# Kernel optimization log

Hardware: AMD Instinct MI355X
Metric: run time of the kernel (lower is better)

## Reference

```python
import jax, jax.numpy as jnp
import numpy as np

B, T, D = 2, 2048, 2048
H = 16
NOPE, ROPE = 128, 64
Q_HEAD = NOPE + ROPE            # 192
Q_LORA = H * Q_HEAD // 4        # 768
KV_RANK = 512
V_DIM = 128
EPS = 1e-6


def setup_inputs() -> dict:
    key = jax.random.key(0)
    ks = jax.random.split(key, 8)
    s = lambda k, shape: jax.random.normal(k, shape, dtype=jnp.float32) * (1.0 / np.sqrt(shape[0]))
    return {
        "hidden_states": jax.random.normal(ks[0], (B, T, D), dtype=jnp.float32),
        "positions": jnp.broadcast_to(jnp.arange(T, dtype=jnp.int64 if jax.config.jax_enable_x64 else jnp.int32), (B, T)),
        "w_qa": s(ks[1], (D, Q_LORA)),
        "g_qa": jnp.ones((Q_LORA,), jnp.float32),
        "w_qb": s(ks[2], (Q_LORA, H * Q_HEAD)),
        "w_kva": s(ks[3], (D, KV_RANK + ROPE)),
        "g_kva": jnp.ones((KV_RANK,), jnp.float32),
        "w_kvb": s(ks[4], (KV_RANK, H * (NOPE + V_DIM))),
        "w_o": s(ks[5], (H * V_DIM, D)),
    }


def _rms(x, g):
    return x * jax.lax.rsqrt(jnp.mean(x * x, axis=-1, keepdims=True) + EPS) * g


def _rotate_half(x):
    h = x.shape[-1] // 2
    return jnp.concatenate([-x[..., h:], x[..., :h]], axis=-1)


def _rope_tables(n):
    inv_freq = 1.0 / (10000.0 ** (jnp.arange(0, ROPE, 2, dtype=jnp.float32) / ROPE))
    freqs = jnp.arange(n, dtype=jnp.float32)[:, None] * inv_freq[None, :]
    emb = jnp.concatenate([freqs, freqs], axis=-1)  # [n, ROPE]
    return jnp.cos(emb), jnp.sin(emb)


def reference(hidden_states, positions, w_qa, g_qa, w_qb, w_kva, g_kva, w_kvb, w_o):
    Bq, Tq, _ = hidden_states.shape
    # Q: low-rank down-proj + RMSNorm + up-proj
    q = _rms(hidden_states @ w_qa, g_qa) @ w_qb
    q = q.reshape(Bq, Tq, H, Q_HEAD)
    q_nope, q_rope = q[..., :NOPE], q[..., NOPE:]
    # KV compression (prefill: no past cache, S == T)
    kvc = hidden_states @ w_kva
    new_c_kv = _rms(kvc[..., :KV_RANK], g_kva)     # [B,S,rank]
    new_k_rope = kvc[..., KV_RANK:]                # [B,S,ROPE]
    S = new_c_kv.shape[1]
    kv = (new_c_kv @ w_kvb).reshape(Bq, S, H, NOPE + V_DIM)
    k_nope, v = kv[..., :NOPE], kv[..., NOPE:]
    # Decoupled RoPE on the rope sub-dimension only
    cos_full, sin_full = _rope_tables(S)
    cos_q = cos_full[positions][:, :, None, :]     # [B,T,1,ROPE]
    sin_q = sin_full[positions][:, :, None, :]
    q_rope = q_rope * cos_q + _rotate_half(q_rope) * sin_q
    cos_k = cos_full[None, :, :]                   # [1,S,ROPE] (all_positions = arange(S))
    sin_k = sin_full[None, :, :]
    k_rope = new_k_rope * cos_k + _rotate_half(new_k_rope) * sin_k  # [B,S,ROPE], shared across heads
    # Assemble full q/k, attention
    q_full = jnp.concatenate([q_nope, q_rope], axis=-1).transpose(0, 2, 1, 3)  # [B,H,T,192]
    k_full = jnp.concatenate(
        [k_nope, jnp.broadcast_to(k_rope[:, :, None, :], (Bq, S, H, ROPE))], axis=-1
    ).transpose(0, 2, 1, 3)                                                     # [B,H,S,192]
    v = v.transpose(0, 2, 1, 3)                                                 # [B,H,S,Vd]
    scale = Q_HEAD ** -0.5
    attn = jnp.einsum("bhtd,bhsd->bhts", q_full, k_full) * scale
    row = jnp.arange(Tq)[:, None]
    col = jnp.arange(S)[None, :]
    attn = jnp.where(col > row + (S - Tq), -jnp.inf, attn)
    attn = jax.nn.softmax(attn, axis=-1)
    out = jnp.einsum("bhts,bhsd->bhtd", attn, v)
    out = out.transpose(0, 2, 1, 3).reshape(Bq, Tq, H * V_DIM)
    output = out @ w_o
    return output, new_c_kv, new_k_rope
```

## Files before the change

### kernel.cpp

```cpp
#include <hip/hip_runtime.h>
#include <stdint.h>

typedef unsigned short ushort_t;
typedef ushort_t u16x8 __attribute__((ext_vector_type(8)));
typedef short s16x8 __attribute__((ext_vector_type(8)));
typedef float f32x4 __attribute__((ext_vector_type(4)));

#define B_ 2
#define T_ 2048
#define D_ 2048
#define H_ 16
#define NOPE_ 128
#define ROPE_ 64
#define QHEAD_ 192
#define QLORA_ 768
#define KVRANK_ 512
#define VDIM_ 128
#define MROWS (B_*T_)
#define KVCW 640

#define MAGIC_F32  0x3F800000u
#define MAGIC_BF16 0x3F803F80u

#define QK_SCALE 0.07216878364870323f

__device__ __forceinline__ float bf2f(ushort_t u) {
    return __uint_as_float(((uint32_t)u) << 16);
}
__device__ __forceinline__ ushort_t f2bf(float f) {
    uint32_t x = __float_as_uint(f);
    x += 0x7fffu + ((x >> 16) & 1u);
    return (ushort_t)(x >> 16);
}
__device__ __forceinline__ float ldf(const float* p) { return *p; }
__device__ __forceinline__ float ldf(const ushort_t* p) { return bf2f(*p); }
__device__ __forceinline__ void stf(float* p, float v) { *p = v; }
__device__ __forceinline__ void stf(ushort_t* p, float v) { *p = f2bf(v); }

__device__ __forceinline__ void load8(const float* p, float* d) {
    float4 a = *(const float4*)p;
    float4 b = *(const float4*)(p + 4);
    d[0]=a.x; d[1]=a.y; d[2]=a.z; d[3]=a.w;
    d[4]=b.x; d[5]=b.y; d[6]=b.z; d[7]=b.w;
}
__device__ __forceinline__ void load8(const ushort_t* p, float* d) {
    u16x8 v = *(const u16x8*)p;
#pragma unroll
    for (int j = 0; j < 8; j++) d[j] = bf2f(v[j]);
}

__device__ __forceinline__ void async_ld16(const ushort_t* g, ushort_t* l) {
    __builtin_amdgcn_global_load_lds(
        (const __attribute__((address_space(1))) void*)g,
        (__attribute__((address_space(3))) void*)l, 16, 0, 0);
}

template <typename OutT>
__launch_bounds__(256)
__global__ void gemm_mfma(const uint32_t* __restrict__ probe, uint32_t magic,
                          const ushort_t* __restrict__ A,
                          const ushort_t* __restrict__ BT,
                          OutT* __restrict__ C, int M, int N, int K) {
    if (magic && *probe != magic) return;

    __shared__ ushort_t As[128 * 32];
    __shared__ ushort_t Bs[128 * 32];

    const int tid = threadIdx.x;
    const int lane = tid & 63;
    const int n16 = lane & 15, quad = lane >> 4;
    const int m0 = blockIdx.y * 128, n0 = blockIdx.x * 128;
    const int w = tid >> 6;
    const int wm = (w & 1) * 64, wn = (w >> 1) * 64;

    f32x4 acc[4][4];
#pragma unroll
    for (int i = 0; i < 4; i++)
#pragma unroll
        for (int j = 0; j < 4; j++) acc[i][j] = (f32x4){0.f, 0.f, 0.f, 0.f};

    const int wbase = tid & ~63;
    for (int kt = 0; kt < K; kt += 32) {
        __syncthreads();
#pragma unroll
        for (int iss = 0; iss < 2; iss++) {
            const int chunk = iss * 256 + tid;
            const int row = chunk >> 2, col = (chunk & 3) * 8;
            const int lbase = (iss * 256 + wbase) * 8;
            async_ld16(A + (long)(m0 + row) * K + kt + col, &As[lbase]);
            async_ld16(BT + (long)(n0 + row) * K + kt + col, &Bs[lbase]);
        }
        __syncthreads();

        s16x8 af[4], bf[4];
#pragma unroll
        for (int i = 0; i < 4; i++) {
            af[i] = *(const s16x8*)&As[(wm + i * 16 + n16) * 32 + quad * 8];
            bf[i] = *(const s16x8*)&Bs[(wn + i * 16 + n16) * 32 + quad * 8];
        }
#pragma unroll
        for (int i = 0; i < 4; i++)
#pragma unroll
            for (int j = 0; j < 4; j++)
                acc[i][j] = __builtin_amdgcn_mfma_f32_16x16x32_bf16(af[i], bf[j], acc[i][j], 0, 0, 0);
    }

#pragma unroll
    for (int i = 0; i < 4; i++) {
        const long mrow = m0 + wm + i * 16 + quad * 4;
#pragma unroll
        for (int j = 0; j < 4; j++) {
            const int nc = n0 + wn + j * 16 + n16;
#pragma unroll
            for (int r = 0; r < 4; r++)
                stf(&C[(mrow + r) * N + nc], acc[i][j][r]);
        }
    }
}

__launch_bounds__(256)
__global__ void gemm_kv_k(const ushort_t* __restrict__ A,
                          const ushort_t* __restrict__ BT,
                          ushort_t* __restrict__ kvK,
                          ushort_t* __restrict__ vTm,
                          int M, int N, int K) {
    __shared__ ushort_t As[128 * 32];
    __shared__ ushort_t Bs[128 * 32];

    const int tid = threadIdx.x;
    const int lane = tid & 63;
    const int n16 = lane & 15, quad = lane >> 4;
    const int m0 = blockIdx.y * 128, n0 = blockIdx.x * 128;
    const int w = tid >> 6;
    const int wm = (w & 1) * 64, wn = (w >> 1) * 64;

    f32x4 acc[4][4];
#pragma unroll
    for (int i = 0; i < 4; i++)
#pragma unroll
        for (int j = 0; j < 4; j++) acc[i][j] = (f32x4){0.f, 0.f, 0.f, 0.f};

    const int wbase = tid & ~63;
    for (int kt = 0; kt < K; kt += 32) {
        __syncthreads();
#pragma unroll
        for (int iss = 0; iss < 2; iss++) {
            const int chunk = iss * 256 + tid;
            const int row = chunk >> 2, col = (chunk & 3) * 8;
            const int lbase = (iss * 256 + wbase) * 8;
            async_ld16(A + (long)(m0 + row) * K + kt + col, &As[lbase]);
            async_ld16(BT + (long)(n0 + row) * K + kt + col, &Bs[lbase]);
        }
        __syncthreads();

        s16x8 af[4], bf[4];
#pragma unroll
        for (int i = 0; i < 4; i++) {
            af[i] = *(const s16x8*)&As[(wm + i * 16 + n16) * 32 + quad * 8];
            bf[i] = *(const s16x8*)&Bs[(wn + i * 16 + n16) * 32 + quad * 8];
        }
#pragma unroll
        for (int i = 0; i < 4; i++)
#pragma unroll
            for (int j = 0; j < 4; j++)
                acc[i][j] = __builtin_amdgcn_mfma_f32_16x16x32_bf16(af[i], bf[j], acc[i][j], 0, 0, 0);
    }

    const bool isV = (n0 & 128) != 0;
#pragma unroll
    for (int i = 0; i < 4; i++) {
        const long mrowb = m0 + wm + i * 16 + quad * 4;
#pragma unroll
        for (int j = 0; j < 4; j++) {
            const int nc = n0 + wn + j * 16 + n16;
            const int hh = nc >> 8, dd = nc & 127;
            if (!isV) {
#pragma unroll
                for (int r = 0; r < 4; r++)
                    kvK[(mrowb + r) * (H_ * NOPE_) + hh * NOPE_ + dd] = f2bf(acc[i][j][r]);
            } else {
#pragma unroll
                for (int r = 0; r < 4; r++) {
                    const long mrow = mrowb + r;
                    const long bb = mrow >> 11, ss = mrow & (T_ - 1);
                    vTm[((bb * H_ + hh) * VDIM_ + dd) * (long)T_ + ss] = f2bf(acc[i][j][r]);
                }
            }
        }
    }
}

template <typename T>
__launch_bounds__(256)
__global__ void cvt_trans_k(const uint32_t* __restrict__ probe, uint32_t magic,
                            const T* __restrict__ src, ushort_t* __restrict__ dst,
                            int K, int N, int NP, float scl) {
    if (*probe != magic) return;
    __shared__ float tile[32][33];
    const int kb = blockIdx.y * 32, nb = blockIdx.x * 32;
    const int tx = threadIdx.x & 31, ty = threadIdx.x >> 5;
#pragma unroll
    for (int i = 0; i < 32; i += 8) {
        const int n = nb + tx;
        tile[ty + i][tx] = (n < N) ? ldf(&src[(long)(kb + ty + i) * N + n]) : 0.f;
    }
    __syncthreads();
#pragma unroll
    for (int i = 0; i < 32; i += 8) {
        const int n = nb + ty + i;
        if (n < NP) dst[(long)n * K + kb + tx] = f2bf(tile[tx][ty + i] * scl);
    }
}

template <typename T>
__launch_bounds__(256)
__global__ void cvt_copy_k(const uint32_t* __restrict__ probe, uint32_t magic,
                           const T* __restrict__ src, ushort_t* __restrict__ dst,
                           long n) {
    if (*probe != magic) return;
    const long i = ((long)blockIdx.x * 256 + threadIdx.x) * 8;
    if (i + 8 <= n) {
        float v[8];
        load8(src + i, v);
        u16x8 o;
#pragma unroll
        for (int j = 0; j < 8; j++) o[j] = f2bf(v[j]);
        *(u16x8*)(dst + i) = o;
    }
}

template <typename GT>
__launch_bounds__(256)
__global__ void rms_k(const uint32_t* __restrict__ probe, uint32_t magic,
                      const float* __restrict__ in, const GT* __restrict__ g,
                      ushort_t* __restrict__ out, int C) {
    if (*probe != magic) return;
    const int row = blockIdx.x;
    const int tid = threadIdx.x;
    const float* ir = in + (long)row * C;

    float ss = 0.f;
    for (int c = tid; c < C; c += 256) { float x = ir[c]; ss += x * x; }
    __shared__ float red[256];
    red[tid] = ss;
    __syncthreads();
    for (int s = 128; s > 0; s >>= 1) {
        if (tid < s) red[tid] += red[tid + s];
        __syncthreads();
    }
    const float inv = rsqrtf(red[0] / (float)C + 1e-6f);
    for (int c = tid; c < C; c += 256)
        out[(long)row * C + c] = f2bf(ir[c] * inv * ldf(&g[c]));
}

template <typename GT, typename OT>
__launch_bounds__(256)
__global__ void rms2_k(const uint32_t* __restrict__ probe, uint32_t magic,
                       const float* __restrict__ in, const GT* __restrict__ g,
                       OT* __restrict__ out_ckv, ushort_t* __restrict__ ckv_i) {
    if (*probe != magic) return;
    const int row = blockIdx.x;
    const int tid = threadIdx.x;
    const float* ir = in + (long)row * KVCW;

    float ss = 0.f;
    for (int c = tid; c < KVRANK_; c += 256) { float x = ir[c]; ss += x * x; }
    __shared__ float red[256];
    red[tid] = ss;
    __syncthreads();
    for (int s = 128; s > 0; s >>= 1) {
        if (tid < s) red[tid] += red[tid + s];
        __syncthreads();
    }
    const float inv = rsqrtf(red[0] / (float)KVRANK_ + 1e-6f);
    for (int c = tid; c < KVRANK_; c += 256) {
        const float v = ir[c] * inv * ldf(&g[c]);
        stf(&out_ckv[(long)row * KVRANK_ + c], v);
        ckv_i[(long)row * KVRANK_ + c] = f2bf(v);
    }
}

template <typename OT>
__launch_bounds__(256)
__global__ void rope_k_k(const uint32_t* __restrict__ probe, uint32_t magic,
                         const float* __restrict__ kvc,
                         OT* __restrict__ out_kr,
                         ushort_t* __restrict__ krope_rot) {
    if (*probe != magic) return;
    const int w = threadIdx.x >> 6, lane = threadIdx.x & 63;
    const int row = blockIdx.x * 4 + w;
    const int t = row & (T_ - 1);
    const float* src = kvc + (long)row * KVCW + KVRANK_;

    const float x = src[lane];
    const float other = src[lane ^ 32];
    const int fi = lane & 31;
    const float inv_freq = exp2f((float)fi * (-13.287712379549449f / 32.f));
    const float ang = (float)t * inv_freq;
    float sn, cs;
    sincosf(ang, &sn, &cs);
    const float rot = (lane < 32) ? -other : other;

    stf(&out_kr[(long)row * ROPE_ + lane], x);
    krope_rot[(long)row * ROPE_ + lane] = f2bf(x * cs + rot * sn);
}

__launch_bounds__(256)
__global__ void rope_q_k(ushort_t* __restrict__ q) {
    const int w = threadIdx.x >> 6, lane = threadIdx.x & 63;
    const int idx = blockIdx.x * 4 + w;
    const int h = idx & (H_ - 1);
    const int row = idx >> 4;
    const int t = row & (T_ - 1);
    ushort_t* qr = q + (long)row * (H_ * QHEAD_) + h * QHEAD_ + NOPE_;

    const float x = bf2f(qr[lane]);
    const float other = bf2f(qr[lane ^ 32]);
    const int fi = lane & 31;
    const float inv_freq = exp2f((float)fi * (-13.287712379549449f / 32.f));
    const float ang = (float)t * inv_freq;
    float sn, cs;
    sincosf(ang, &sn, &cs);
    const float rot = (lane < 32) ? -other : other;
    qr[lane] = f2bf(x * cs + rot * sn);
}

#define BQ 64
#define BK 64
#define PSTR 68

__launch_bounds__(256, 2)
__global__ void attn_mfma_k(const ushort_t* __restrict__ q,
                            const ushort_t* __restrict__ kvK,
                            const ushort_t* __restrict__ vTm,
                            const ushort_t* __restrict__ krope,
                            ushort_t* __restrict__ attn_out) {
    __shared__ ushort_t ks[2][BK * 192];
    __shared__ ushort_t ps[4][16][PSTR];

    const int tid = threadIdx.x;
    const int w = tid >> 6, lane = tid & 63;
    const int n16 = lane & 15, quad = lane >> 4;

    const int L = (int)blockIdx.x;
    const int slot = L >> 3;
    const int bhg = slot >> 5;
    const int qts = slot & 31;
    const int bh = (L & 7) | (bhg << 3);
    const int qt = (bhg & 1) ? (31 - qts) : qts;
    const int h = bh & (H_ - 1), b = bh >> 4;

    const int q0 = qt * BQ;
    const int qw = q0 + w * 16;

    s16x8 qf[6];
    {
        const ushort_t* qrow = q + (long)(b * T_ + qw + n16) * (H_ * QHEAD_) + h * QHEAD_;
#pragma unroll
        for (int c = 0; c < 6; c++)
            qf[c] = *(const s16x8*)(qrow + c * 32 + quad * 8);
    }

    s16x8 kones;
#pragma unroll
    for (int j = 0; j < 8; j++) kones[j] = (short)0x3F80;

    f32x4 O[8];
#pragma unroll
    for (int f = 0; f < 8; f++) O[f] = (f32x4){0.f, 0.f, 0.f, 0.f};
    float mrow[4], lrow[4];
#pragma unroll
    for (int r = 0; r < 4; r++) { mrow[r] = -3.0e38f; lrow[r] = 0.f; }

    const int ntiles = qt + 1;

    const ushort_t* spb[6];  int sstr[6];
#pragma unroll
    for (int i = 0; i < 6; i++) {
        const int off = w * 6144 + i * 1024 + lane * 16;
        const int row = off / 384;
        const int c16 = (off % 384) >> 4;
        const int csrc = c16 ^ (row & 7);
        if (csrc < 16) {
            spb[i] = kvK + (long)(b * T_ + row) * (H_ * NOPE_) + h * NOPE_ + csrc * 8;
            sstr[i] = H_ * NOPE_;
        } else {
            spb[i] = krope + (long)(b * T_ + row) * ROPE_ + (csrc - 16) * 8;
            sstr[i] = ROPE_;
        }
    }

    const ushort_t* vbase = vTm + ((long)bh * VDIM_ + n16) * T_ + quad * 8;
    const int r7 = n16 & 7;

#pragma unroll
    for (int i = 0; i < 6; i++)
        async_ld16(spb[i], &ks[0][w * 3072 + i * 512]);

    int cur = 0;
    for (int kt = 0; kt < ntiles; kt++) {
        const int s0 = kt * BK;
        const int sn = (kt + 1 < ntiles ? kt + 1 : kt) * BK;

        s16x8 vb[2][8];
#pragma unroll
        for (int kc = 0; kc < 2; kc++)
#pragma unroll
            for (int vt = 0; vt < 8; vt++)
                vb[kc][vt] = *(const s16x8*)(vbase + (long)(vt * 16) * T_ + s0 + kc * 32);
        __builtin_amdgcn_sched_barrier(0);

        asm volatile("s_waitcnt vmcnt(16)" ::: "memory");
        __builtin_amdgcn_s_barrier();
        __builtin_amdgcn_sched_barrier(0);

#pragma unroll
        for (int i = 0; i < 6; i++)
            async_ld16(spb[i] + (long)sn * sstr[i], &ks[cur ^ 1][w * 3072 + i * 512]);
        __builtin_amdgcn_sched_barrier(0);

        const ushort_t* kb = &ks[cur][0];
        f32x4 Sc[4];
        __builtin_amdgcn_s_setprio(1);
#pragma unroll
        for (int st = 0; st < 4; st++) {
            Sc[st] = (f32x4){0.f, 0.f, 0.f, 0.f};
            const int row = st * 16 + n16;
            const int rbase = row * 192;
#pragma unroll
            for (int c = 0; c < 4; c++) {
                s16x8 bfr = *(const s16x8*)&kb[rbase + (((4 * c + quad) ^ r7) << 3)];
                Sc[st] = __builtin_amdgcn_mfma_f32_16x16x32_bf16(qf[c], bfr, Sc[st], 0, 0, 0);
            }
#pragma unroll
            for (int c2 = 0; c2 < 2; c2++) {
                s16x8 bfr = *(const s16x8*)&kb[rbase + (((16 + 4 * c2 + quad) ^ r7) << 3)];
                Sc[st] = __builtin_amdgcn_mfma_f32_16x16x32_bf16(qf[4 + c2], bfr, Sc[st], 0, 0, 0);
            }
        }
        __builtin_amdgcn_s_setprio(0);

        const bool diag = (s0 + BK > q0);
        float Sv[4][4];
#pragma unroll
        for (int st = 0; st < 4; st++) {
            const int sg = s0 + st * 16 + n16;
#pragma unroll
            for (int r = 0; r < 4; r++) {
                float v = Sc[st][r];
                if (diag && sg > qw + quad * 4 + r) v = -3.0e38f;
                Sv[st][r] = v;
            }
        }

        float rmx[4];
#pragma unroll
        for (int r = 0; r < 4; r++)
            rmx[r] = fmaxf(fmaxf(Sv[0][r], Sv[1][r]), fmaxf(Sv[2][r], Sv[3][r]));

        bool ok = true;
#pragma unroll
        for (int r = 0; r < 4; r++) ok = ok && (rmx[r] <= mrow[r] + 8.0f);
        if (!__all(ok)) {
            float mnew[4], alpha[4];
#pragma unroll
            for (int r = 0; r < 4; r++) {
                float mx = rmx[r];
#pragma unroll
                for (int off = 8; off > 0; off >>= 1)
                    mx = fmaxf(mx, __shfl_xor(mx, off, 64));
                mnew[r] = fmaxf(mrow[r], mx);
                alpha[r] = __expf(mrow[r] - mnew[r]);
                mrow[r] = mnew[r];
                lrow[r] *= alpha[r];
            }
#pragma unroll
            for (int f = 0; f < 8; f++)
#pragma unroll
                for (int r = 0; r < 4; r++) O[f][r] *= alpha[r];
        }

#pragma unroll
        for (int st = 0; st < 4; st++)
#pragma unroll
            for (int r = 0; r < 4; r++)
                ps[w][quad * 4 + r][st * 16 + n16] = f2bf(__expf(Sv[st][r] - mrow[r]));

        asm volatile("s_waitcnt vmcnt(6)" ::: "memory");
        __builtin_amdgcn_sched_barrier(0);

        f32x4 sacc = (f32x4){0.f, 0.f, 0.f, 0.f};
        __builtin_amdgcn_s_setprio(1);
#pragma unroll
        for (int kc = 0; kc < 2; kc++) {
            s16x8 afr = *(const s16x8*)&ps[w][n16][kc * 32 + quad * 8];
            sacc = __builtin_amdgcn_mfma_f32_16x16x32_bf16(afr, kones, sacc, 0, 0, 0);
#pragma unroll
            for (int vt = 0; vt < 8; vt++)
                O[vt] = __builtin_amdgcn_mfma_f32_16x16x32_bf16(afr, vb[kc][vt], O[vt], 0, 0, 0);
        }
        __builtin_amdgcn_s_setprio(0);
#pragma unroll
        for (int r = 0; r < 4; r++) lrow[r] += sacc[r];

        cur ^= 1;
    }

    float linv[4];
#pragma unroll
    for (int r = 0; r < 4; r++) linv[r] = 1.f / lrow[r];
    ushort_t* obase = attn_out + (long)(b * T_ + qw) * (H_ * VDIM_) + h * VDIM_;
#pragma unroll
    for (int vt = 0; vt < 8; vt++)
#pragma unroll
        for (int r = 0; r < 4; r++)
            obase[(long)(quad * 4 + r) * (H_ * VDIM_) + vt * 16 + n16] =
                f2bf(O[vt][r] * linv[r]);
}

extern "C" void kernel_launch(void* const* d_in, const int* in_sizes, int n_in,
                              void* d_out, int out_size, void* d_ws, size_t ws_size,
                              hipStream_t stream) {
    const uint32_t* probe = (const uint32_t*)d_in[3];

    char* ws = (char*)d_ws;
    ushort_t* q      = (ushort_t*)ws;
    ushort_t* hs_b   = (ushort_t*)ws;
    ushort_t* woT    = (ushort_t*)ws;
    ushort_t* kvK    = (ushort_t*)(ws + 25165824);
    ushort_t* vTm    = (ushort_t*)(ws + 41943040);
    float*    qlr    = (float*)(ws + 25165824);
    float*    kvc    = (float*)(ws + 37748736);
    ushort_t* wqaT   = (ushort_t*)(ws + 48234496);
    ushort_t* wqbT   = (ushort_t*)(ws + 48234496);
    ushort_t* wkvaT  = (ushort_t*)(ws + 51380224);
    ushort_t* attn_i = (ushort_t*)(ws + 58720256);
    ushort_t* ckv_i  = (ushort_t*)(ws + 58720256);
    ushort_t* qln    = (ushort_t*)(ws + 62914560);
    ushort_t* wkvbT  = (ushort_t*)(ws + 69206016);
    ushort_t* krope  = (ushort_t*)(ws + 76283904 - 786432);

    const float* hs_f  = (const float*)d_in[0];
    const float* wqa_f = (const float*)d_in[2];
    const float* gqa_f = (const float*)d_in[3];
    const float* wqb_f = (const float*)d_in[4];
    const float* wkva_f= (const float*)d_in[5];
    const float* gkva_f= (const float*)d_in[6];
    const float* wkvb_f= (const float*)d_in[7];
    const float* wo_f  = (const float*)d_in[8];
    float* oy_f  = (float*)d_out;
    float* ock_f = oy_f + (long)MROWS * D_;
    float* okr_f = ock_f + (long)MROWS * KVRANK_;

    const ushort_t* hs_h  = (const ushort_t*)d_in[0];
    const ushort_t* wqa_h = (const ushort_t*)d_in[2];
    const ushort_t* gqa_h = (const ushort_t*)d_in[3];
    const ushort_t* wqb_h = (const ushort_t*)d_in[4];
    const ushort_t* wkva_h= (const ushort_t*)d_in[5];
    const ushort_t* gkva_h= (const ushort_t*)d_in[6];
    const ushort_t* wkvb_h= (const ushort_t*)d_in[7];
    const ushort_t* wo_h  = (const ushort_t*)d_in[8];
    ushort_t* oy_h  = (ushort_t*)d_out;
    ushort_t* ock_h = oy_h + (long)MROWS * D_;
    ushort_t* okr_h = ock_h + (long)MROWS * KVRANK_;

    const dim3 blk(256);

    cvt_copy_k<float><<<4096, blk, 0, stream>>>(probe, MAGIC_F32, hs_f, hs_b, (long)MROWS * D_);
    cvt_copy_k<ushort_t><<<4096, blk, 0, stream>>>(probe, MAGIC_BF16, hs_h, hs_b, (long)MROWS * D_);
    cvt_trans_k<float><<<dim3(24, 64), blk, 0, stream>>>(probe, MAGIC_F32, wqa_f, wqaT, D_, QLORA_, QLORA_, 1.f);
    cvt_trans_k<ushort_t><<<dim3(24, 64), blk, 0, stream>>>(probe, MAGIC_BF16, wqa_h, wqaT, D_, QLORA_, QLORA_, 1.f);
    cvt_trans_k<float><<<dim3(20, 64), blk, 0, stream>>>(probe, MAGIC_F32, wkva_f, wkvaT, D_, KVRANK_ + ROPE_, KVCW, 1.f);
    cvt_trans_k<ushort_t><<<dim3(20, 64), blk, 0, stream>>>(probe, MAGIC_BF16, wkva_h, wkvaT, D_, KVRANK_ + ROPE_, KVCW, 1.f);

    gemm_mfma<float><<<dim3(QLORA_ / 128, MROWS / 128), blk, 0, stream>>>(probe, 0u, hs_b, wqaT, qlr, MROWS, QLORA_, D_);
    gemm_mfma<float><<<dim3(KVCW / 128, MROWS / 128), blk, 0, stream>>>(probe, 0u, hs_b, wkvaT, kvc, MROWS, KVCW, D_);

    rms_k<float><<<MROWS, blk, 0, stream>>>(probe, MAGIC_F32, qlr, gqa_f, qln, QLORA_);
    rms_k<ushort_t><<<MROWS, blk, 0, stream>>>(probe, MAGIC_BF16, qlr, gqa_h, qln, QLORA_);
    rms2_k<float, float><<<MROWS, blk, 0, stream>>>(probe, MAGIC_F32, kvc, gkva_f, ock_f, ckv_i);
    rms2_k<ushort_t, ushort_t><<<MROWS, blk, 0, stream>>>(probe, MAGIC_BF16, kvc, gkva_h, ock_h, ckv_i);
    rope_k_k<float><<<MROWS / 4, blk, 0, stream>>>(probe, MAGIC_F32, kvc, okr_f, krope);
    rope_k_k<ushort_t><<<MROWS / 4, blk, 0, stream>>>(probe, MAGIC_BF16, kvc, okr_h, krope);

    cvt_trans_k<float><<<dim3(96, 24), blk, 0, stream>>>(probe, MAGIC_F32, wqb_f, wqbT, QLORA_, H_ * QHEAD_, H_ * QHEAD_, QK_SCALE);
    cvt_trans_k<ushort_t><<<dim3(96, 24), blk, 0, stream>>>(probe, MAGIC_BF16, wqb_h, wqbT, QLORA_, H_ * QHEAD_, H_ * QHEAD_, QK_SCALE);
    gemm_mfma<ushort_t><<<dim3((H_ * QHEAD_) / 128, MROWS / 128), blk, 0, stream>>>(probe, 0u, qln, wqbT, q, MROWS, H_ * QHEAD_, QLORA_);

    cvt_trans_k<float><<<dim3(128, 16), blk, 0, stream>>>(probe, MAGIC_F32, wkvb_f, wkvbT, KVRANK_, H_ * 256, H_ * 256, 1.f);
    cvt_trans_k<ushort_t><<<dim3(128, 16), blk, 0, stream>>>(probe, MAGIC_BF16, wkvb_h, wkvbT, KVRANK_, H_ * 256, H_ * 256, 1.f);
    gemm_kv_k<<<dim3((H_ * 256) / 128, MROWS / 128), blk, 0, stream>>>(ckv_i, wkvbT, kvK, vTm, MROWS, H_ * 256, KVRANK_);

    rope_q_k<<<(MROWS * H_) / 4, blk, 0, stream>>>(q);
    attn_mfma_k<<<dim3(B_ * H_ * (T_ / BQ)), blk, 0, stream>>>(q, kvK, vTm, krope, attn_i);

    cvt_trans_k<float><<<dim3(64, 64), blk, 0, stream>>>(probe, MAGIC_F32, wo_f, woT, H_ * VDIM_, D_, D_, 1.f);
    cvt_trans_k<ushort_t><<<dim3(64, 64), blk, 0, stream>>>(probe, MAGIC_BF16, wo_h, woT, H_ * VDIM_, D_, D_, 1.f);
    gemm_mfma<float><<<dim3(D_ / 128, MROWS / 128), blk, 0, stream>>>(probe, MAGIC_F32, attn_i, woT, oy_f, MROWS, D_, H_ * VDIM_);
    gemm_mfma<ushort_t><<<dim3(D_ / 128, MROWS / 128), blk, 0, stream>>>(probe, MAGIC_BF16, attn_i, woT, oy_h, MROWS, D_, H_ * VDIM_);
}
```

Baseline: 580.6 us.

## Halve attention key tile to 32, raise occupancy, skip fully masked per-wave tiles

The flash-attention kernel now walks keys in 32-wide tiles instead of 64, halving LDS for K and P. Launch bounds allow 4 blocks per CU instead of 2. Each wave skips the QK, softmax and PV work for tiles that lie entirely above its causal diagonal. The P scratch buffer gets an XOR swizzle in place of padding. The cost is twice as many loop iterations and barriers per block, plus more register pressure under the tighter occupancy target.

Result: slower. 798.0 us (+37.4%).

```diff
diff --git a/kernel.cpp b/kernel.cpp
--- a/kernel.cpp
+++ b/kernel.cpp
@@ -326,17 +326,16 @@
 }
 
 #define BQ 64
-#define BK 64
-#define PSTR 68
-
-__launch_bounds__(256, 2)
+#define BK 32
+
+__launch_bounds__(256, 4)
 __global__ void attn_mfma_k(const ushort_t* __restrict__ q,
                             const ushort_t* __restrict__ kvK,
                             const ushort_t* __restrict__ vTm,
                             const ushort_t* __restrict__ krope,
                             ushort_t* __restrict__ attn_out) {
     __shared__ ushort_t ks[2][BK * 192];
-    __shared__ ushort_t ps[4][16][PSTR];
+    __shared__ ushort_t ps[4][16][32];
 
     const int tid = threadIdx.x;
     const int w = tid >> 6, lane = tid & 63;
@@ -372,12 +371,12 @@
 #pragma unroll
     for (int r = 0; r < 4; r++) { mrow[r] = -3.0e38f; lrow[r] = 0.f; }
 
-    const int ntiles = qt + 1;
-
-    const ushort_t* spb[6];  int sstr[6];
-#pragma unroll
-    for (int i = 0; i < 6; i++) {
-        const int off = w * 6144 + i * 1024 + lane * 16;
+    const int ntiles = 2 * qt + 2;
+
+    const ushort_t* spb[3];  int sstr[3];
+#pragma unroll
+    for (int i = 0; i < 3; i++) {
+        const int off = w * 3072 + i * 1024 + lane * 16;
         const int row = off / 384;
         const int c16 = (off % 384) >> 4;
         const int csrc = c16 ^ (row & 7);
@@ -392,116 +391,121 @@
 
     const ushort_t* vbase = vTm + ((long)bh * VDIM_ + n16) * T_ + quad * 8;
     const int r7 = n16 & 7;
-
-#pragma unroll
-    for (int i = 0; i < 6; i++)
-        async_ld16(spb[i], &ks[0][w * 3072 + i * 512]);
+    const int p3 = n16 & 3;
+
+#pragma unroll
+    for (int i = 0; i < 3; i++)
+        async_ld16(spb[i], &ks[0][w * 1536 + i * 512]);
 
     int cur = 0;
     for (int kt = 0; kt < ntiles; kt++) {
         const int s0 = kt * BK;
         const int sn = (kt + 1 < ntiles ? kt + 1 : kt) * BK;
-
-        s16x8 vb[2][8];
-#pragma unroll
-        for (int kc = 0; kc < 2; kc++)
-#pragma unroll
-            for (int vt = 0; vt < 8; vt++)
-                vb[kc][vt] = *(const s16x8*)(vbase + (long)(vt * 16) * T_ + s0 + kc * 32);
+        const bool active = (s0 <= qw + 15);
+
+        s16x8 vb[8];
+#pragma unroll
+        for (int vt = 0; vt < 8; vt++)
+            vb[vt] = *(const s16x8*)(vbase + (long)(vt * 16) * T_ + s0);
         __builtin_amdgcn_sched_barrier(0);
 
-        asm volatile("s_waitcnt vmcnt(16)" ::: "memory");
+        asm volatile("s_waitcnt vmcnt(8)" ::: "memory");
         __builtin_amdgcn_s_barrier();
         __builtin_amdgcn_sched_barrier(0);
 
 #pragma unroll
-        for (int i = 0; i < 6; i++)
-            async_ld16(spb[i] + (long)sn * sstr[i], &ks[cur ^ 1][w * 3072 + i * 512]);
+        for (int i = 0; i < 3; i++)
+            async_ld16(spb[i] + (long)sn * sstr[i], &ks[cur ^ 1][w * 1536 + i * 512]);
         __builtin_amdgcn_sched_barrier(0);
 
-        const ushort_t* kb = &ks[cur][0];
-        f32x4 Sc[4];
-        __builtin_amdgcn_s_setprio(1);
-#pragma unroll
-        for (int st = 0; st < 4; st++) {
-            Sc[st] = (f32x4){0.f, 0.f, 0.f, 0.f};
-            const int row = st * 16 + n16;
-            const int rbase = row * 192;
-#pragma unroll
-            for (int c = 0; c < 4; c++) {
-                s16x8 bfr = *(const s16x8*)&kb[rbase + (((4 * c + quad) ^ r7) << 3)];
-                Sc[st] = __builtin_amdgcn_mfma_f32_16x16x32_bf16(qf[c], bfr, Sc[st], 0, 0, 0);
+        float Sv[2][4];
+        if (active) {
+            const ushort_t* kb = &ks[cur][0];
+            f32x4 Sc[2];
+            __builtin_amdgcn_s_setprio(1);
+#pragma unroll
+            for (int st = 0; st < 2; st++) {
+                Sc[st] = (f32x4){0.f, 0.f, 0.f, 0.f};
+                const int row = st * 16 + n16;
+                const int rbase = row * 192;
+#pragma unroll
+                for (int c = 0; c < 4; c++) {
+                    s16x8 bfr = *(const s16x8*)&kb[rbase + (((4 * c + quad) ^ r7) << 3)];
+                    Sc[st] = __builtin_amdgcn_mfma_f32_16x16x32_bf16(qf[c], bfr, Sc[st], 0, 0, 0);
+                }
+#pragma unroll
+                for (int c2 = 0; c2 < 2; c2++) {
+                    s16x8 bfr = *(const s16x8*)&kb[rbase + (((16 + 4 * c2 + quad) ^ r7) << 3)];
+                    Sc[st] = __builtin_amdgcn_mfma_f32_16x16x32_bf16(qf[4 + c2], bfr, Sc[st], 0, 0, 0);
+                }
             }
-#pragma unroll
-            for (int c2 = 0; c2 < 2; c2++) {
-                s16x8 bfr = *(const s16x8*)&kb[rbase + (((16 + 4 * c2 + quad) ^ r7) << 3)];
-                Sc[st] = __builtin_amdgcn_mfma_f32_16x16x32_bf16(qf[4 + c2], bfr, Sc[st], 0, 0, 0);
+            __builtin_amdgcn_s_setprio(0);
+
+            const bool diag = (s0 + BK > q0);
+#pragma unroll
+            for (int st = 0; st < 2; st++) {
+                const int sg = s0 + st * 16 + n16;
+#pragma unroll
+                for (int r = 0; r < 4; r++) {
+                    float v = Sc[st][r];
+                    if (diag && sg > qw + quad * 4 + r) v = -3.0e38f;
+                    Sv[st][r] = v;
+                }
             }
-        }
-        __builtin_amdgcn_s_setprio(0);
-
-        const bool diag = (s0 + BK > q0);
-        float Sv[4][4];
-#pragma unroll
-        for (int st = 0; st < 4; st++) {
-            const int sg = s0 + st * 16 + n16;
-#pragma unroll
-            for (int r = 0; r < 4; r++) {
-                float v = Sc[st][r];
-                if (diag && sg > qw + quad * 4 + r) v = -3.0e38f;
-                Sv[st][r] = v;
+
+            float rmx[4];
+#pragma unroll
+            for (int r = 0; r < 4; r++)
+                rmx[r] = fmaxf(Sv[0][r], Sv[1][r]);
+
+            bool ok = true;
+#pragma unroll
+            for (int r = 0; r < 4; r++) ok = ok && (rmx[r] <= mrow[r] + 8.0f);
+            if (!__all(ok)) {
+                float alpha[4];
+#pragma unroll
+                for (int r = 0; r < 4; r++) {
+                    float mx = rmx[r];
+#pragma unroll
+                    for (int off = 8; off > 0; off >>= 1)
+                        mx = fmaxf(mx, __shfl_xor(mx, off, 64));
+                    const float mnew = fmaxf(mrow[r], mx);
+                    alpha[r] = __expf(mrow[r] - mnew);
+                    mrow[r] = mnew;
+                    lrow[r] *= alpha[r];
+                }
+#pragma unroll
+                for (int f = 0; f < 8; f++)
+#pragma unroll
+                    for (int r = 0; r < 4; r++) O[f][r] *= alpha[r];
             }
-        }
-
-        float rmx[4];
-#pragma unroll
-        for (int r = 0; r < 4; r++)
-            rmx[r] = fmaxf(fmaxf(Sv[0][r], Sv[1][r]), fmaxf(Sv[2][r], Sv[3][r]));
-
-        bool ok = true;
-#pragma unroll
-        for (int r = 0; r < 4; r++) ok = ok && (rmx[r] <= mrow[r] + 8.0f);
-        if (!__all(ok)) {
-            float mnew[4], alpha[4];
-#pragma unroll
-            for (int r = 0; r < 4; r++) {
-                float mx = rmx[r];
-#pragma unroll
-                for (int off = 8; off > 0; off >>= 1)
-                    mx = fmaxf(mx, __shfl_xor(mx, off, 64));
-                mnew[r] = fmaxf(mrow[r], mx);
-                alpha[r] = __expf(mrow[r] - mnew[r]);
-                mrow[r] = mnew[r];
-                lrow[r] *= alpha[r];
-            }
-#pragma unroll
-            for (int f = 0; f < 8; f++)
-#pragma unroll
-                for (int r = 0; r < 4; r++) O[f][r] *= alpha[r];
-        }
-
-#pragma unroll
-        for (int st = 0; st < 4; st++)
-#pragma unroll
-            for (int r = 0; r < 4; r++)
-                ps[w][quad * 4 + r][st * 16 + n16] = f2bf(__expf(Sv[st][r] - mrow[r]));
-
-        asm volatile("s_waitcnt vmcnt(6)" ::: "memory");
+
+#pragma unroll
+            for (int st = 0; st < 2; st++)
+#pragma unroll
+                for (int r = 0; r < 4; r++) {
+                    const int row_w = quad * 4 + r;
+                    const int chunk = (st * 2 + (n16 >> 3)) ^ (row_w & 3);
+                    ps[w][row_w][(chunk << 3) | (n16 & 7)] =
+                        f2bf(__expf(Sv[st][r] - mrow[r]));
+                }
+        }
+
+        asm volatile("s_waitcnt vmcnt(3)" ::: "memory");
         __builtin_amdgcn_sched_barrier(0);
 
-        f32x4 sacc = (f32x4){0.f, 0.f, 0.f, 0.f};
-        __builtin_amdgcn_s_setprio(1);
-#pragma unroll
-        for (int kc = 0; kc < 2; kc++) {
-            s16x8 afr = *(const s16x8*)&ps[w][n16][kc * 32 + quad * 8];
+        if (active) {
+            f32x4 sacc = (f32x4){0.f, 0.f, 0.f, 0.f};
+            __builtin_amdgcn_s_setprio(1);
+            s16x8 afr = *(const s16x8*)&ps[w][n16][(quad ^ p3) << 3];
             sacc = __builtin_amdgcn_mfma_f32_16x16x32_bf16(afr, kones, sacc, 0, 0, 0);
 #pragma unroll
             for (int vt = 0; vt < 8; vt++)
-                O[vt] = __builtin_amdgcn_mfma_f32_16x16x32_bf16(afr, vb[kc][vt], O[vt], 0, 0, 0);
-        }
-        __builtin_amdgcn_s_setprio(0);
-#pragma unroll
-        for (int r = 0; r < 4; r++) lrow[r] += sacc[r];
+                O[vt] = __builtin_amdgcn_mfma_f32_16x16x32_bf16(afr, vb[vt], O[vt], 0, 0, 0);
+            __builtin_amdgcn_s_setprio(0);
+#pragma unroll
+            for (int r = 0; r < 4; r++) lrow[r] += sacc[r];
+        }
 
         cur ^= 1;
     }
```
